# Optimization experiments

Measured on AMD Instinct MI355X. Metric: run time of the kernel, lower is better.

The kernel has to match this reference:

```python
import jax, jax.numpy as jnp
import numpy as np

N, M, D = 16384, 4096, 512
TEMP = 1.0


def setup_inputs() -> dict:
    key = jax.random.key(0)
    kx, ky = jax.random.split(key)
    x = jax.random.normal(kx, (N, D), dtype=jnp.float32)
    y = jax.random.normal(ky, (M, D), dtype=jnp.float32)
    return {"x": x, "y": y, "temperature": 1}


def reference(x, y, temperature):
    # euclidean_distances_logits:
    #   logits = -0.5 * T * sum_d (x[n,None,:] - y[None,m,:])**2
    # Fused form avoiding the O(n*m*d) broadcast intermediate (same math):
    t = jnp.asarray(temperature, dtype=x.dtype) * jnp.float32(TEMP)
    x_sq = jnp.sum(x * x, axis=1, keepdims=True)          # [n, 1]
    y_sq = jnp.sum(y * y, axis=1)[None, :]                # [1, m]
    xy = jnp.einsum("nd,md->nm", x, y)                    # [n, m]
    sq_dist = x_sq - 2.0 * xy + y_sq                      # [n, m]
    return -0.5 * t * sq_dist
```

## Files before the change

### kernel.cpp

```cpp
#include <hip/hip_runtime.h>
#include <hip/hip_bf16.h>


#define NN 16384
#define MM 4096
#define DD 512

using frag_ab = __attribute__((ext_vector_type(8))) short;
using floatx4 = __attribute__((ext_vector_type(4))) float;

__device__ __forceinline__ unsigned bf16rne(float f) {
    union { float f; unsigned u; } v; v.f = f;
    unsigned u = v.u + 0x7FFFu + ((v.u >> 16) & 1u);
    return u >> 16;
}

__device__ __forceinline__ uint2 cvt4(float4 v) {
    uint2 r;
    r.x = bf16rne(v.x) | (bf16rne(v.y) << 16);
    r.y = bf16rne(v.z) | (bf16rne(v.w) << 16);
    return r;
}

__global__ void rowsq_kernel(const float* __restrict__ v, float* __restrict__ sq) {
    const int lane = threadIdx.x & 63;
    const int row  = blockIdx.x * 4 + (threadIdx.x >> 6);
    const float* p = v + (size_t)row * DD + lane * 8;
    float4 a = *(const float4*)(p);
    float4 b = *(const float4*)(p + 4);
    float s = a.x*a.x + a.y*a.y + a.z*a.z + a.w*a.w
            + b.x*b.x + b.y*b.y + b.z*b.z + b.w*b.w;
    #pragma unroll
    for (int off = 32; off > 0; off >>= 1) s += __shfl_xor(s, off);
    if (lane == 0) sq[row] = s;
}

__global__ __launch_bounds__(256) void protonet_gemm(
    const float* __restrict__ x, const float* __restrict__ y,
    const float* __restrict__ xsq, const float* __restrict__ ysq,
    const int* __restrict__ temp, float* __restrict__ out)
{
    __shared__ __align__(16) unsigned short As[128 * 32];
    __shared__ __align__(16) unsigned short Bs[128 * 32];

    const int bn   = blockIdx.x;
    const int bm   = blockIdx.y;
    const int tid  = threadIdx.x;
    const int lane = tid & 63;
    const int wave = tid >> 6;
    const int wn   = wave & 1;
    const int wm   = wave >> 1;
    const int l15  = lane & 15;
    const int quad = lane >> 4;

    floatx4 acc[4][4] = {};

    for (int k0 = 0; k0 < DD; k0 += 32) {
        #pragma unroll
        for (int i = 0; i < 4; ++i) {
            int c = tid + i * 256;
            int row = c >> 3, col4 = c & 7;
            float4 v = *(const float4*)(x + (size_t)(bn * 128 + row) * DD + k0 + col4 * 4);
            *(uint2*)(&As[row * 32 + col4 * 4]) = cvt4(v);
        }
        #pragma unroll
        for (int i = 0; i < 4; ++i) {
            int c = tid + i * 256;
            int row = c >> 3, col4 = c & 7;
            float4 v = *(const float4*)(y + (size_t)(bm * 128 + row) * DD + k0 + col4 * 4);
            *(uint2*)(&Bs[row * 32 + col4 * 4]) = cvt4(v);
        }
        __syncthreads();

        frag_ab a[4], b[4];
        #pragma unroll
        for (int t = 0; t < 4; ++t) {
            a[t] = *(const frag_ab*)(&As[(wn * 64 + t * 16 + l15) * 32 + quad * 8]);
            b[t] = *(const frag_ab*)(&Bs[(wm * 64 + t * 16 + l15) * 32 + quad * 8]);
        }
        #pragma unroll
        for (int tn = 0; tn < 4; ++tn)
            #pragma unroll
            for (int tm = 0; tm < 4; ++tm)
                acc[tn][tm] = __builtin_amdgcn_mfma_f32_16x16x32_bf16(
                    a[tn], b[tm], acc[tn][tm], 0, 0, 0);
        __syncthreads();
    }

    const float t = (float)(*temp);
    const int n_base = bn * 128 + wn * 64;
    const int m_base = bm * 128 + wm * 64;
    #pragma unroll
    for (int tn = 0; tn < 4; ++tn) {
        float xs[4];
        #pragma unroll
        for (int r = 0; r < 4; ++r) xs[r] = xsq[n_base + tn * 16 + quad * 4 + r];
        #pragma unroll
        for (int tm = 0; tm < 4; ++tm) {
            const int mcol = m_base + tm * 16 + l15;
            const float ys = ysq[mcol];
            #pragma unroll
            for (int r = 0; r < 4; ++r) {
                const int nrow = n_base + tn * 16 + quad * 4 + r;
                out[(size_t)nrow * MM + mcol] = t * (acc[tn][tm][r] - 0.5f * (xs[r] + ys));
            }
        }
    }
}

extern "C" void kernel_launch(void* const* d_in, const int* in_sizes, int n_in,
                              void* d_out, int out_size, void* d_ws, size_t ws_size,
                              hipStream_t stream) {
    const float* x    = (const float*)d_in[0];
    const float* y    = (const float*)d_in[1];
    const int*   temp = (const int*)d_in[2];
    float* out = (float*)d_out;
    float* xsq = (float*)d_ws;
    float* ysq = xsq + NN;

    rowsq_kernel<<<NN / 4, 256, 0, stream>>>(x, xsq);
    rowsq_kernel<<<MM / 4, 256, 0, stream>>>(y, ysq);
    protonet_gemm<<<dim3(NN / 128, MM / 128), 256, 0, stream>>>(x, y, xsq, ysq, temp, out);
}
```

Before: 451.0 us.

## Pre-convert inputs to bf16 and stream GEMM tiles via global_load_lds

```diff
diff --git a/kernel.cpp b/kernel.cpp
--- a/kernel.cpp
+++ b/kernel.cpp
@@ -8,6 +8,13 @@
 
 using frag_ab = __attribute__((ext_vector_type(8))) short;
 using floatx4 = __attribute__((ext_vector_type(4))) float;
+
+using gas_ptr = const __attribute__((address_space(1))) void*;
+using las_ptr = __attribute__((address_space(3))) void*;
+
+__device__ __forceinline__ void async_copy16(const void* g, void* l) {
+    __builtin_amdgcn_global_load_lds((gas_ptr)g, (las_ptr)l, 16, 0, 0);
+}
 
 __device__ __forceinline__ unsigned bf16rne(float f) {
     union { float f; unsigned u; } v; v.f = f;
@@ -20,6 +27,22 @@
     r.x = bf16rne(v.x) | (bf16rne(v.y) << 16);
     r.y = bf16rne(v.z) | (bf16rne(v.w) << 16);
     return r;
+}
+
+__global__ void prep_kernel(const float* __restrict__ v, float* __restrict__ sq,
+                            unsigned short* __restrict__ vb) {
+    const int lane = threadIdx.x & 63;
+    const int row  = blockIdx.x * 4 + (threadIdx.x >> 6);
+    const float* p = v + (size_t)row * DD + lane * 8;
+    float4 a = *(const float4*)(p);
+    float4 b = *(const float4*)(p + 4);
+    uint2 lo = cvt4(a), hi = cvt4(b);
+    *(uint4*)(vb + (size_t)row * DD + lane * 8) = make_uint4(lo.x, lo.y, hi.x, hi.y);
+    float s = a.x*a.x + a.y*a.y + a.z*a.z + a.w*a.w
+            + b.x*b.x + b.y*b.y + b.z*b.z + b.w*b.w;
+    #pragma unroll
+    for (int off = 32; off > 0; off >>= 1) s += __shfl_xor(s, off);
+    if (lane == 0) sq[row] = s;
 }
 
 __global__ void rowsq_kernel(const float* __restrict__ v, float* __restrict__ sq) {
@@ -35,8 +58,8 @@
     if (lane == 0) sq[row] = s;
 }
 
-__global__ __launch_bounds__(256) void protonet_gemm(
-    const float* __restrict__ x, const float* __restrict__ y,
+__global__ __launch_bounds__(256) void protonet_gemm_bf(
+    const unsigned short* __restrict__ xb, const unsigned short* __restrict__ yb,
     const float* __restrict__ xsq, const float* __restrict__ ysq,
     const int* __restrict__ temp, float* __restrict__ out)
 {
@@ -55,6 +78,74 @@
 
     floatx4 acc[4][4] = {};
 
+    const unsigned short* ga0 = xb + (size_t)(bn * 128 + (wave * 2 + 0) * 16 + l15) * DD + quad * 8;
+    const unsigned short* ga1 = xb + (size_t)(bn * 128 + (wave * 2 + 1) * 16 + l15) * DD + quad * 8;
+    const unsigned short* gb0 = yb + (size_t)(bm * 128 + (wave * 2 + 0) * 16 + l15) * DD + quad * 8;
+    const unsigned short* gb1 = yb + (size_t)(bm * 128 + (wave * 2 + 1) * 16 + l15) * DD + quad * 8;
+
+    for (int k0 = 0; k0 < DD; k0 += 32) {
+        async_copy16(ga0 + k0, As + (wave * 2 + 0) * 512);
+        async_copy16(ga1 + k0, As + (wave * 2 + 1) * 512);
+        async_copy16(gb0 + k0, Bs + (wave * 2 + 0) * 512);
+        async_copy16(gb1 + k0, Bs + (wave * 2 + 1) * 512);
+        __syncthreads();
+
+        frag_ab a[4], b[4];
+        #pragma unroll
+        for (int t = 0; t < 4; ++t) {
+            a[t] = *(const frag_ab*)(As + (wn * 4 + t) * 512 + lane * 8);
+            b[t] = *(const frag_ab*)(Bs + (wm * 4 + t) * 512 + lane * 8);
+        }
+        #pragma unroll
+        for (int tn = 0; tn < 4; ++tn)
+            #pragma unroll
+            for (int tm = 0; tm < 4; ++tm)
+                acc[tn][tm] = __builtin_amdgcn_mfma_f32_16x16x32_bf16(
+                    a[tn], b[tm], acc[tn][tm], 0, 0, 0);
+        __syncthreads();
+    }
+
+    const float t = (float)(*temp);
+    const int n_base = bn * 128 + wn * 64;
+    const int m_base = bm * 128 + wm * 64;
+    #pragma unroll
+    for (int tn = 0; tn < 4; ++tn) {
+        float xs[4];
+        #pragma unroll
+        for (int r = 0; r < 4; ++r) xs[r] = xsq[n_base + tn * 16 + quad * 4 + r];
+        #pragma unroll
+        for (int tm = 0; tm < 4; ++tm) {
+            const int mcol = m_base + tm * 16 + l15;
+            const float ys = ysq[mcol];
+            #pragma unroll
+            for (int r = 0; r < 4; ++r) {
+                const int nrow = n_base + tn * 16 + quad * 4 + r;
+                out[(size_t)nrow * MM + mcol] = t * (acc[tn][tm][r] - 0.5f * (xs[r] + ys));
+            }
+        }
+    }
+}
+
+__global__ __launch_bounds__(256) void protonet_gemm(
+    const float* __restrict__ x, const float* __restrict__ y,
+    const float* __restrict__ xsq, const float* __restrict__ ysq,
+    const int* __restrict__ temp, float* __restrict__ out)
+{
+    __shared__ __align__(16) unsigned short As[128 * 32];
+    __shared__ __align__(16) unsigned short Bs[128 * 32];
+
+    const int bn   = blockIdx.x;
+    const int bm   = blockIdx.y;
+    const int tid  = threadIdx.x;
+    const int lane = tid & 63;
+    const int wave = tid >> 6;
+    const int wn   = wave & 1;
+    const int wm   = wave >> 1;
+    const int l15  = lane & 15;
+    const int quad = lane >> 4;
+
+    floatx4 acc[4][4] = {};
+
     for (int k0 = 0; k0 < DD; k0 += 32) {
         #pragma unroll
         for (int i = 0; i < 4; ++i) {
@@ -115,10 +206,23 @@
     const float* y    = (const float*)d_in[1];
     const int*   temp = (const int*)d_in[2];
     float* out = (float*)d_out;
+
     float* xsq = (float*)d_ws;
     float* ysq = xsq + NN;
-
-    rowsq_kernel<<<NN / 4, 256, 0, stream>>>(x, xsq);
-    rowsq_kernel<<<MM / 4, 256, 0, stream>>>(y, ysq);
-    protonet_gemm<<<dim3(NN / 128, MM / 128), 256, 0, stream>>>(x, y, xsq, ysq, temp, out);
-}
+    unsigned short* xb = (unsigned short*)(ysq + MM);
+    unsigned short* yb = xb + (size_t)NN * DD;
+
+    const size_t need = (size_t)(NN + MM) * 4 + (size_t)(NN + MM) * DD * 2;
+
+    if (ws_size >= need) {
+        prep_kernel<<<NN / 4, 256, 0, stream>>>(x, xsq, xb);
+        prep_kernel<<<MM / 4, 256, 0, stream>>>(y, ysq, yb);
+        protonet_gemm_bf<<<dim3(NN / 128, MM / 128), 256, 0, stream>>>(
+            xb, yb, xsq, ysq, temp, out);
+    } else {
+        rowsq_kernel<<<NN / 4, 256, 0, stream>>>(x, xsq);
+        rowsq_kernel<<<MM / 4, 256, 0, stream>>>(y, ysq);
+        protonet_gemm<<<dim3(NN / 128, MM / 128), 256, 0, stream>>>(
+            x, y, xsq, ysq, temp, out);
+    }
+}
```

After: 419.5 us. 7.0% less time.
